# Performance work log

Hardware: AMD Instinct MI355X
Metric: run time of the kernel (lower is better)

The kernel has to match this reference:

```python
import jax, jax.numpy as jnp
import numpy as np

DIM = 1024
HEADS = 16
HEAD_DIM = DIM // HEADS
HIDDEN = int(DIM * 4.0)
EPS = 1e-5


def layernorm(x, w, b):
    m = jnp.mean(x, axis=-1, keepdims=True)
    v = jnp.var(x, axis=-1, keepdims=True)
    return (x - m) * jax.lax.rsqrt(v + EPS) * w + b


def apply_rope(t, pos):
    # t: [B, H, S, D], pos: [B, S] int
    half = t.shape[-1] // 2
    inv_freq = 1.0 / (10000.0 ** (jnp.arange(half, dtype=jnp.float32) / half))
    ang = pos.astype(jnp.float32)[:, None, :, None] * inv_freq  # [B,1,S,half]
    cos = jnp.cos(ang)
    sin = jnp.sin(ang)
    t1, t2 = t[..., :half], t[..., half:]
    return jnp.concatenate([t1 * cos - t2 * sin, t2 * cos + t1 * sin], axis=-1)


def setup_inputs() -> dict:
    key = jax.random.key(0)
    ks = jax.random.split(key, 10)
    B, S = 2, 2048
    x = jax.random.normal(ks[0], (B, S, DIM), dtype=jnp.float32)
    pos = jnp.sort(jax.random.randint(ks[1], (B, S), 0, 2048), axis=-1).astype(jnp.int32)
    def lin(k, fi, fo):
        return jax.random.normal(k, (fi, fo), dtype=jnp.float32) / np.sqrt(fi)
    return {
        "x": x,
        "pos": pos,
        "ln1_w": jnp.ones((DIM,), jnp.float32),
        "ln1_b": jnp.zeros((DIM,), jnp.float32),
        "qkv_w": lin(ks[2], DIM, 3 * DIM),
        "qkv_b": jnp.zeros((3 * DIM,), jnp.float32),
        "o_w": lin(ks[3], DIM, DIM),
        "o_b": jnp.zeros((DIM,), jnp.float32),
        "ln2_w": jnp.ones((DIM,), jnp.float32),
        "ln2_b": jnp.zeros((DIM,), jnp.float32),
        "mlp_w1": lin(ks[4], DIM, HIDDEN),
        "mlp_b1": jnp.zeros((HIDDEN,), jnp.float32),
        "mlp_w2": lin(ks[5], HIDDEN, DIM),
        "mlp_b2": jnp.zeros((DIM,), jnp.float32),
    }


def reference(x, pos, ln1_w, ln1_b, qkv_w, qkv_b, o_w, o_b, ln2_w, ln2_b, mlp_w1, mlp_b1, mlp_w2, mlp_b2):
    B, S, C = x.shape
    scale = HEAD_DIM ** -0.5
    xn = layernorm(x, ln1_w, ln1_b)
    qkv = (xn @ qkv_w + qkv_b).reshape(B, S, 3, HEADS, HEAD_DIM)
    qkv = jnp.transpose(qkv, (2, 0, 3, 1, 4))  # [3,B,H,S,D]
    q, k, v = qkv[0], qkv[1], qkv[2]
    q = apply_rope(q, pos)
    k = apply_rope(k, pos)
    scores = jnp.einsum("bhsd,bhtd->bhst", q, k) * scale
    probs = jax.nn.softmax(scores, axis=-1)
    attn = jnp.einsum("bhst,bhtd->bhsd", probs, v)
    attn = jnp.transpose(attn, (0, 2, 1, 3)).reshape(B, S, C)
    x = x + attn @ o_w + o_b
    xn2 = layernorm(x, ln2_w, ln2_b)
    h = jax.nn.gelu(xn2 @ mlp_w1 + mlp_b1, approximate=False)
    x = x + h @ mlp_w2 + mlp_b2
    return x
```

## Files before the change

### kernel.cpp

```cpp
#include <hip/hip_runtime.h>
#include <hip/hip_bf16.h>
#include <math.h>

#define DIMC 1024
#define HEADS 16
#define HD 64
#define HIDDEN 4096
#define BATCH 2
#define SEQ 2048
#define TOK (BATCH*SEQ)

typedef unsigned short u16;
typedef __attribute__((ext_vector_type(8))) short short8;
typedef __attribute__((ext_vector_type(4))) float f32x4;

__device__ __forceinline__ u16 f2bf(float f) {
  unsigned u = __float_as_uint(f);
  u += 0x7fff + ((u >> 16) & 1);
  return (u16)(u >> 16);
}
__device__ __forceinline__ float bf2f(u16 h) {
  return __uint_as_float(((unsigned)h) << 16);
}

__device__ __forceinline__ void gl_lds16(const void* g, void* l) {
  __builtin_amdgcn_global_load_lds(
      (__attribute__((address_space(1))) void*)g,
      (__attribute__((address_space(3))) void*)l, 16, 0, 0);
}

__device__ __forceinline__ const short8* lds_row128(const u16* base, int row, int chunk) {
  return (const short8*)((const char*)base + row * 128 + (((chunk) ^ (row & 7)) << 4));
}

__global__ __launch_bounds__(256) void ln_kernel(
    const float* __restrict__ x, const float* __restrict__ w,
    const float* __restrict__ b, u16* __restrict__ out)
{
  int row = blockIdx.x, tid = threadIdx.x;
  const float4* xr = (const float4*)(x + (size_t)row * DIMC);
  float4 v = xr[tid];
  float s = v.x + v.y + v.z + v.w;
  float s2 = v.x*v.x + v.y*v.y + v.z*v.z + v.w*v.w;
  for (int off = 32; off > 0; off >>= 1) {
    s  += __shfl_down(s, off);
    s2 += __shfl_down(s2, off);
  }
  __shared__ float red[8];
  int lane = tid & 63, wv = tid >> 6;
  if (lane == 0) { red[wv] = s; red[4 + wv] = s2; }
  __syncthreads();
  float S  = red[0] + red[1] + red[2] + red[3];
  float S2 = red[4] + red[5] + red[6] + red[7];
  float mean = S * (1.f / DIMC);
  float var  = S2 * (1.f / DIMC) - mean * mean;
  float inv  = rsqrtf(var + 1e-5f);
  int base = tid * 4;
  float vv[4] = {v.x, v.y, v.z, v.w};
#pragma unroll
  for (int j = 0; j < 4; ++j)
    out[(size_t)row * DIMC + base + j] = f2bf((vv[j] - mean) * inv * w[base + j] + b[base + j]);
}

__global__ __launch_bounds__(256) void transpose_cast(
    const float* __restrict__ W, u16* __restrict__ Wt, int K, int N)
{
  __shared__ float t[32][33];
  int n0 = blockIdx.x * 32, k0 = blockIdx.y * 32;
  for (int r = threadIdx.y; r < 32; r += 8)
    t[r][threadIdx.x] = W[(size_t)(k0 + r) * N + n0 + threadIdx.x];
  __syncthreads();
  for (int r = threadIdx.y; r < 32; r += 8)
    Wt[(size_t)(n0 + r) * K + k0 + threadIdx.x] = f2bf(t[threadIdx.x][r]);
}

__device__ __forceinline__ void grid_map(int BM, int& m0, int& n0) {
  int gx = gridDim.x, gy = gridDim.y;
  int nwg = gx * gy;
  int orig = blockIdx.y * gx + blockIdx.x;
  int wg = (orig & 7) * (nwg >> 3) + (orig >> 3);
  int bx = wg / gy, by = wg - bx * gy;
  m0 = by * BM;
  n0 = bx * 128;
}

template<int GELU>
__device__ __forceinline__ void gemm_lin_body(
    u16* shm, const u16* __restrict__ A, const u16* __restrict__ Bt,
    const float* __restrict__ bias, u16* __restrict__ outb, int M, int N, int K)
{
  int tid = threadIdx.x;
  int lane = tid & 63, w = tid >> 6;
  int wr = w >> 1, wc = w & 1;
  int m0, n0;
  grid_map(128, m0, n0);

  f32x4 acc[4][4] = {};

  int offA[4], offB[4];
#pragma unroll
  for (int j = 0; j < 4; ++j) {
    int p = tid + j * 256, row = p >> 3, cl = (p & 7) ^ (row & 7);
    offA[j] = (m0 + row) * K + cl * 8;
    offB[j] = (n0 + row) * K + cl * 8;
  }
  int rofs = lane & 15, q4 = lane >> 4;
  int NT = K >> 6;
  u16* Bs = shm + 128 * 64;

  for (int t = 0; t < NT; ++t) {
#pragma unroll
    for (int j = 0; j < 4; ++j) {
      gl_lds16(A + offA[j] + t * 64, shm + (tid + j * 256) * 8);
      gl_lds16(Bt + offB[j] + t * 64, Bs + (tid + j * 256) * 8);
    }
    __syncthreads();
    {
      short8 af[4][2], bfr[4][2];
#pragma unroll
      for (int mm = 0; mm < 4; ++mm)
#pragma unroll
        for (int kk = 0; kk < 2; ++kk) {
          int row = wr * 64 + mm * 16 + rofs;
          af[mm][kk] = *(const short8*)((const char*)shm + row * 128 +
                                        ((((kk << 2) | q4) ^ (row & 7)) << 4));
        }
#pragma unroll
      for (int nn = 0; nn < 4; ++nn)
#pragma unroll
        for (int kk = 0; kk < 2; ++kk) {
          int row = wc * 64 + nn * 16 + rofs;
          bfr[nn][kk] = *(const short8*)((const char*)Bs + row * 128 +
                                         ((((kk << 2) | q4) ^ (row & 7)) << 4));
        }
#pragma unroll
      for (int kk = 0; kk < 2; ++kk)
#pragma unroll
        for (int mm = 0; mm < 4; ++mm)
#pragma unroll
          for (int nn = 0; nn < 4; ++nn)
            acc[mm][nn] = __builtin_amdgcn_mfma_f32_16x16x32_bf16(
                af[mm][kk], bfr[nn][kk], acc[mm][nn], 0, 0, 0);
    }
    __syncthreads();
  }

  u16* C = shm;
#pragma unroll
  for (int nn = 0; nn < 4; ++nn) {
    int ccol = wc * 64 + nn * 16 + rofs;
    float bv = bias[n0 + ccol];
#pragma unroll
    for (int mm = 0; mm < 4; ++mm)
#pragma unroll
      for (int r = 0; r < 4; ++r) {
        int crow = wr * 64 + mm * 16 + q4 * 4 + r;
        float v = acc[mm][nn][r] + bv;
        if (GELU) v = 0.5f * v * (1.f + erff(v * 0.70710678118f));
        C[crow * 128 + ccol] = f2bf(v);
      }
  }
  __syncthreads();
  for (int c = tid; c < 128 * 16; c += 256) {
    int row = c >> 4, off = (c & 15) * 8;
    *(short8*)(outb + (size_t)(m0 + row) * N + n0 + off) = *(const short8*)&C[row * 128 + off];
  }
}

__global__ __launch_bounds__(256) void gemm_qkv(
    const u16* __restrict__ A, const u16* __restrict__ Bt,
    const float* __restrict__ bias, u16* __restrict__ outb, int M, int N, int K)
{
  __shared__ u16 shm[128 * 64 * 2];
  gemm_lin_body<0>(shm, A, Bt, bias, outb, M, N, K);
}
__global__ __launch_bounds__(256) void gemm_mlp1(
    const u16* __restrict__ A, const u16* __restrict__ Bt,
    const float* __restrict__ bias, u16* __restrict__ outb, int M, int N, int K)
{
  __shared__ u16 shm[128 * 64 * 2];
  gemm_lin_body<1>(shm, A, Bt, bias, outb, M, N, K);
}

__device__ __forceinline__ void gemm_res_body(
    u16* shm, const u16* __restrict__ A, const u16* __restrict__ Bt,
    const float* __restrict__ bias, const float* __restrict__ res,
    float* __restrict__ outf, int M, int N, int K)
{
  constexpr int BM = 64, AMM = 2, HALF = 32, AJ = 2;
  constexpr int ASZ = BM * 64, BSZ = 128 * 64;
  int tid = threadIdx.x;
  int lane = tid & 63, w = tid >> 6;
  int wr = w >> 1, wc = w & 1;
  int m0, n0;
  grid_map(BM, m0, n0);

  f32x4 acc[AMM][4] = {};

  int offA[AJ], offB[4];
#pragma unroll
  for (int j = 0; j < AJ; ++j) {
    int p = tid + j * 256, row = p >> 3, cl = (p & 7) ^ (row & 7);
    offA[j] = (m0 + row) * K + cl * 8;
  }
#pragma unroll
  for (int j = 0; j < 4; ++j) {
    int p = tid + j * 256, row = p >> 3, cl = (p & 7) ^ (row & 7);
    offB[j] = (n0 + row) * K + cl * 8;
  }
  int rofs = lane & 15, q4 = lane >> 4;
  int NT = K >> 6;

  auto stage = [&](int buf, int t) {
    u16* Ab = shm + buf * ASZ;
    u16* Bb = shm + 2 * ASZ + buf * BSZ;
#pragma unroll
    for (int j = 0; j < AJ; ++j)
      gl_lds16(A + offA[j] + t * 64, Ab + (tid + j * 256) * 8);
#pragma unroll
    for (int j = 0; j < 4; ++j)
      gl_lds16(Bt + offB[j] + t * 64, Bb + (tid + j * 256) * 8);
  };
  auto compute = [&](int buf) {
    const char* Ab = (const char*)(shm + buf * ASZ);
    const char* Bb = (const char*)(shm + 2 * ASZ + buf * BSZ);
    short8 af[AMM][2], bfr[4][2];
#pragma unroll
    for (int mm = 0; mm < AMM; ++mm)
#pragma unroll
      for (int kk = 0; kk < 2; ++kk) {
        int row = wr * HALF + mm * 16 + rofs;
        af[mm][kk] = *(const short8*)(Ab + row * 128 +
                                      ((((kk << 2) | q4) ^ (row & 7)) << 4));
      }
#pragma unroll
    for (int nn = 0; nn < 4; ++nn)
#pragma unroll
      for (int kk = 0; kk < 2; ++kk) {
        int row = wc * 64 + nn * 16 + rofs;
        bfr[nn][kk] = *(const short8*)(Bb + row * 128 +
                                       ((((kk << 2) | q4) ^ (row & 7)) << 4));
      }
#pragma unroll
    for (int kk = 0; kk < 2; ++kk)
#pragma unroll
      for (int mm = 0; mm < AMM; ++mm)
#pragma unroll
        for (int nn = 0; nn < 4; ++nn)
          acc[mm][nn] = __builtin_amdgcn_mfma_f32_16x16x32_bf16(
              af[mm][kk], bfr[nn][kk], acc[mm][nn], 0, 0, 0);
  };

  stage(0, 0);
  __syncthreads();
  int cur = 0;
  for (int t = 0; t < NT; ++t) {
    if (t + 1 < NT) stage(cur ^ 1, t + 1);
    compute(cur);
    __syncthreads();
    cur ^= 1;
  }

  float* Cf = (float*)shm;
#pragma unroll
  for (int p = 0; p < 2; ++p) {
    if (wr == p) {
#pragma unroll
      for (int nn = 0; nn < 4; ++nn) {
        int ccol = wc * 64 + nn * 16 + rofs;
        float bv = bias[n0 + ccol];
#pragma unroll
        for (int mm = 0; mm < AMM; ++mm)
#pragma unroll
          for (int r = 0; r < 4; ++r)
            Cf[(mm * 16 + q4 * 4 + r) * 128 + ccol] = acc[mm][nn][r] + bv;
      }
    }
    __syncthreads();
    for (int c = tid; c < HALF * 32; c += 256) {
      int row = c >> 5, off = (c & 31) * 4;
      size_t idx = (size_t)(m0 + p * HALF + row) * N + n0 + off;
      float4 rv = *(const float4*)(res + idx);
      float4 cv = *(const float4*)&Cf[row * 128 + off];
      cv.x += rv.x; cv.y += rv.y; cv.z += rv.z; cv.w += rv.w;
      *(float4*)(outf + idx) = cv;
    }
    __syncthreads();
  }
}

__global__ __launch_bounds__(256) void gemm_oproj(
    const u16* __restrict__ A, const u16* __restrict__ Bt,
    const float* __restrict__ bias, const float* __restrict__ res,
    float* __restrict__ outf, int M, int N, int K)
{
  __shared__ u16 shm[(64 + 128) * 64 * 2];
  gemm_res_body(shm, A, Bt, bias, res, outf, M, N, K);
}
__global__ __launch_bounds__(256) void gemm_mlp2(
    const u16* __restrict__ A, const u16* __restrict__ Bt,
    const float* __restrict__ bias, const float* __restrict__ res,
    float* __restrict__ outf, int M, int N, int K)
{
  __shared__ u16 shm[(64 + 128) * 64 * 2];
  gemm_res_body(shm, A, Bt, bias, res, outf, M, N, K);
}

__global__ __launch_bounds__(256) void rope_split(
    const u16* __restrict__ qkv, const int* __restrict__ pos,
    u16* __restrict__ Q, u16* __restrict__ Kk, u16* __restrict__ Vt)
{
  int st = blockIdx.x, bh = blockIdx.y;
  int b = bh >> 4, hh = bh & 15;
  int s0 = st * 64;
  int tid = threadIdx.x;
  __shared__ u16 vtile[64][72];

  for (int i = tid; i < 64 * 32; i += 256) {
    int sl = i >> 5, dp = i & 31;
    int s = s0 + sl;
    float p = (float)pos[b * SEQ + s];
    float freq = exp2f((float)dp * -0.4152410118609203f);
    float ang = p * freq;
    float sn, c;
    __sincosf(ang, &sn, &c);
    const u16* qr = qkv + (size_t)(b * SEQ + s) * 3072 + hh * 64;
    float q1 = bf2f(qr[dp]),        q2 = bf2f(qr[dp + 32]);
    float k1 = bf2f(qr[1024 + dp]), k2 = bf2f(qr[1024 + dp + 32]);
    size_t ob = ((size_t)bh * SEQ + s) * HD;
    const float QS = 0.18033688011112042f;
    Q[ob + dp]       = f2bf((q1 * c - q2 * sn) * QS);
    Q[ob + dp + 32]  = f2bf((q2 * c + q1 * sn) * QS);
    Kk[ob + dp]      = f2bf(k1 * c - k2 * sn);
    Kk[ob + dp + 32] = f2bf(k2 * c + k1 * sn);
  }
  for (int i = tid; i < 64 * 64; i += 256) {
    int sl = i >> 6, d = i & 63;
    vtile[d][sl] = qkv[(size_t)(b * SEQ + s0 + sl) * 3072 + 2048 + hh * 64 + d];
  }
  __syncthreads();
  for (int i = tid; i < 64 * 64; i += 256) {
    int d = i >> 6, sl = i & 63;
    Vt[((size_t)bh * HD + d) * SEQ + s0 + sl] = vtile[d][sl];
  }
}

__global__ __launch_bounds__(256) void attn128(
    const u16* __restrict__ Q, const u16* __restrict__ K,
    const u16* __restrict__ Vt, u16* __restrict__ O)
{
  __shared__ u16 Ks[2][64 * 64];
  __shared__ u16 Vs[2][64 * 64];
  __shared__ u16 Ps[4 * 32 * 64];
  int orig = blockIdx.y * gridDim.x + blockIdx.x;
  int bh = (orig & 7) * 4 + ((orig >> 3) & 3);
  int qt = orig >> 5;
  int b = bh >> 4, hh = bh & 15;
  const u16* Qp = Q + ((size_t)bh * SEQ + qt * 128) * HD;
  const u16* Kp = K + (size_t)bh * SEQ * HD;
  const u16* Vp = Vt + (size_t)bh * HD * SEQ;
  int tid = threadIdx.x, lane = tid & 63, w = tid >> 6;
  int rofs = lane & 15, q4 = lane >> 4;
  int kofs = q4 * 8;

  short8 aq[2][2];
#pragma unroll
  for (int m = 0; m < 2; ++m)
#pragma unroll
    for (int h = 0; h < 2; ++h)
      aq[m][h] = *(const short8*)&Qp[(m * 64 + w * 16 + rofs) * HD + h * 32 + kofs];

  short8 ones;
#pragma unroll
  for (int j = 0; j < 8; ++j) ones[j] = (short)0x3F80;

  f32x4 o[2][4] = {};
  f32x4 lsum[2] = {};

  int srow = tid >> 3;
  int sg0 = ((tid & 7) ^ (srow & 7)) * 8;
  u16* pw = &Ps[w * 32 * 64];

#define A_STAGE(BUF, T0) do { \
    gl_lds16(Kp + (size_t)((T0) + srow) * HD + sg0, &Ks[BUF][tid * 8]); \
    gl_lds16(Kp + (size_t)((T0) + 32 + srow) * HD + sg0, &Ks[BUF][tid * 8 + 2048]); \
    gl_lds16(Vp + (size_t)srow * SEQ + (T0) + sg0, &Vs[BUF][tid * 8]); \
    gl_lds16(Vp + (size_t)(32 + srow) * SEQ + (T0) + sg0, &Vs[BUF][tid * 8 + 2048]); \
  } while (0)

  auto tile = [&](const u16* KsB, const u16* VsB) {
    f32x4 s[2][4] = {};
    short8 bk0[4], bk1[4];
#pragma unroll
    for (int n = 0; n < 4; ++n) {
      int krow = n * 16 + rofs;
      bk0[n] = *lds_row128(KsB, krow, q4);
      bk1[n] = *lds_row128(KsB, krow, 4 + q4);
    }
#pragma unroll
    for (int m = 0; m < 2; ++m)
#pragma unroll
      for (int n = 0; n < 4; ++n) {
        s[m][n] = __builtin_amdgcn_mfma_f32_16x16x32_bf16(aq[m][0], bk0[n], s[m][n], 0, 0, 0);
        s[m][n] = __builtin_amdgcn_mfma_f32_16x16x32_bf16(aq[m][1], bk1[n], s[m][n], 0, 0, 0);
      }
#pragma unroll
    for (int m = 0; m < 2; ++m)
#pragma unroll
      for (int n = 0; n < 4; ++n)
#pragma unroll
        for (int r = 0; r < 4; ++r) {
          int prow = m * 16 + q4 * 4 + r;
          int pbyte = (n * 16 + rofs) * 2;
          float p = __builtin_amdgcn_exp2f(s[m][n][r]);
          *(u16*)((char*)pw + prow * 128 + (pbyte ^ ((prow & 7) << 4))) = f2bf(p);
        }
    short8 pa[2][2];
#pragma unroll
    for (int m = 0; m < 2; ++m) {
      pa[m][0] = *lds_row128(pw, m * 16 + rofs, q4);
      pa[m][1] = *lds_row128(pw, m * 16 + rofs, 4 + q4);
    }
    short8 bv0[4], bv1[4];
#pragma unroll
    for (int n = 0; n < 4; ++n) {
      int vrow = n * 16 + rofs;
      bv0[n] = *lds_row128(VsB, vrow, q4);
      bv1[n] = *lds_row128(VsB, vrow, 4 + q4);
    }
#pragma unroll
    for (int m = 0; m < 2; ++m) {
      lsum[m] = __builtin_amdgcn_mfma_f32_16x16x32_bf16(pa[m][0], ones, lsum[m], 0, 0, 0);
      lsum[m] = __builtin_amdgcn_mfma_f32_16x16x32_bf16(pa[m][1], ones, lsum[m], 0, 0, 0);
#pragma unroll
      for (int n = 0; n < 4; ++n) {
        o[m][n] = __builtin_amdgcn_mfma_f32_16x16x32_bf16(pa[m][0], bv0[n], o[m][n], 0, 0, 0);
        o[m][n] = __builtin_amdgcn_mfma_f32_16x16x32_bf16(pa[m][1], bv1[n], o[m][n], 0, 0, 0);
      }
    }
  };

  A_STAGE(0, 0);
  __syncthreads();
  for (int t0 = 0; t0 < SEQ; t0 += 128) {
    if (t0 + 64 < SEQ) A_STAGE(1, t0 + 64);
    tile(Ks[0], Vs[0]);
    __syncthreads();
    if (t0 + 128 < SEQ) A_STAGE(0, t0 + 128);
    tile(Ks[1], Vs[1]);
    __syncthreads();
  }
#undef A_STAGE

#pragma unroll
  for (int m = 0; m < 2; ++m)
#pragma unroll
    for (int r = 0; r < 4; ++r) {
      float inv = 1.f / lsum[m][r];
      int rr = m * 64 + w * 16 + q4 * 4 + r;
#pragma unroll
      for (int n = 0; n < 4; ++n)
        Ps[rr * 64 + n * 16 + rofs] = f2bf(o[m][n][r] * inv);
    }
  __syncthreads();
  for (int c = tid; c < 128 * 8; c += 256) {
    int row = c >> 3, off = (c & 7) * 8;
    int sq = qt * 128 + row;
    *(short8*)(O + ((size_t)b * SEQ + sq) * DIMC + hh * 64 + off) = *(const short8*)&Ps[row * 64 + off];
  }
}

extern "C" void kernel_launch(void* const* d_in, const int* in_sizes, int n_in,
                              void* d_out, int out_size, void* d_ws, size_t ws_size,
                              hipStream_t stream) {
  const float* x     = (const float*)d_in[0];
  const int*   pos   = (const int*)  d_in[1];
  const float* ln1_w = (const float*)d_in[2];
  const float* ln1_b = (const float*)d_in[3];
  const float* qkv_w = (const float*)d_in[4];
  const float* qkv_b = (const float*)d_in[5];
  const float* o_w   = (const float*)d_in[6];
  const float* o_b   = (const float*)d_in[7];
  const float* ln2_w = (const float*)d_in[8];
  const float* ln2_b = (const float*)d_in[9];
  const float* w1    = (const float*)d_in[10];
  const float* b1    = (const float*)d_in[11];
  const float* w2    = (const float*)d_in[12];
  const float* b2    = (const float*)d_in[13];
  float* out = (float*)d_out;

  char* ws = (char*)d_ws;
  u16* WqkvT = (u16*)(ws + 0);
  u16* WoT   = (u16*)(ws + 6291456);
  u16* W1T   = (u16*)(ws + 8388608);
  u16* W2T   = (u16*)(ws + 16777216);
  u16* xn    = (u16*)(ws + 25165824);
  u16* qkvbf = (u16*)(ws + 33554432);
  u16* Qb    = (u16*)(ws + 58720256);
  u16* Kb    = (u16*)(ws + 67108864);
  u16* Vtb   = (u16*)(ws + 75497472);
  u16* attnb = (u16*)(ws + 83886080);
  u16* hbuf  = (u16*)(ws + 25165824);
  float* x2  = (float*)(ws + 58720256);
  u16* xn2   = (u16*)(ws + 75497472);

  transpose_cast<<<dim3(3072/32, 1024/32), dim3(32, 8), 0, stream>>>(qkv_w, WqkvT, 1024, 3072);
  transpose_cast<<<dim3(1024/32, 1024/32), dim3(32, 8), 0, stream>>>(o_w,  WoT,  1024, 1024);
  transpose_cast<<<dim3(4096/32, 1024/32), dim3(32, 8), 0, stream>>>(w1,   W1T,  1024, 4096);
  transpose_cast<<<dim3(1024/32, 4096/32), dim3(32, 8), 0, stream>>>(w2,   W2T,  4096, 1024);

  ln_kernel<<<TOK, 256, 0, stream>>>(x, ln1_w, ln1_b, xn);
  gemm_qkv<<<dim3(24, 32), 256, 0, stream>>>(xn, WqkvT, qkv_b, qkvbf, 4096, 3072, 1024);
  rope_split<<<dim3(32, 32), 256, 0, stream>>>(qkvbf, pos, Qb, Kb, Vtb);
  attn128<<<dim3(16, 32), 256, 0, stream>>>(Qb, Kb, Vtb, attnb);
  gemm_oproj<<<dim3(8, 64), 256, 0, stream>>>(attnb, WoT, o_b, x, x2, 4096, 1024, 1024);
  ln_kernel<<<TOK, 256, 0, stream>>>(x2, ln2_w, ln2_b, xn2);
  gemm_mlp1<<<dim3(32, 32), 256, 0, stream>>>(xn2, W1T, b1, hbuf, 4096, 4096, 1024);
  gemm_mlp2<<<dim3(8, 64), 256, 0, stream>>>(hbuf, W2T, b2, x2, out, 4096, 1024, 4096);
}
```

Before: 257.6 us.

## Double-buffer QKV GEMM and retile MLP1 GEMM to 256x256 with 1024 threads

The QKV GEMM now uses double-buffered LDS staging, so the next K-tile's global-to-LDS loads overlap the current tile's MFMA work and one barrier per iteration goes away. The MLP1 GEMM is rewritten as a 1024-thread, 256x256 output tile with K-step 32, double buffering and s_setprio around the MFMA block, and its epilogue is written in two halves through LDS. The larger tile is meant to raise operand reuse and cut global traffic. In exchange LDS use and per-block resources grow, and only 256 blocks are launched, which may fill the CUs poorly.

```diff
diff --git a/kernel.cpp b/kernel.cpp
--- a/kernel.cpp
+++ b/kernel.cpp
@@ -74,26 +74,28 @@
     Wt[(size_t)(n0 + r) * K + k0 + threadIdx.x] = f2bf(t[threadIdx.x][r]);
 }
 
-__device__ __forceinline__ void grid_map(int BM, int& m0, int& n0) {
+__device__ __forceinline__ void grid_map(int BM, int BN, int& m0, int& n0) {
   int gx = gridDim.x, gy = gridDim.y;
   int nwg = gx * gy;
   int orig = blockIdx.y * gx + blockIdx.x;
   int wg = (orig & 7) * (nwg >> 3) + (orig >> 3);
   int bx = wg / gy, by = wg - bx * gy;
   m0 = by * BM;
-  n0 = bx * 128;
-}
-
-template<int GELU>
-__device__ __forceinline__ void gemm_lin_body(
-    u16* shm, const u16* __restrict__ A, const u16* __restrict__ Bt,
-    const float* __restrict__ bias, u16* __restrict__ outb, int M, int N, int K)
-{
+  n0 = bx * BN;
+}
+
+__global__ __launch_bounds__(256) void gemm_qkv(
+    const u16* __restrict__ A, const u16* __restrict__ Bt,
+    const float* __restrict__ bias, u16* __restrict__ outb,
+    int M, int N, int K)
+{
+  constexpr int ASZ = 128 * 64, BSZ = 128 * 64;
+  __shared__ u16 shm[ASZ * 2 + BSZ * 2];
   int tid = threadIdx.x;
   int lane = tid & 63, w = tid >> 6;
   int wr = w >> 1, wc = w & 1;
   int m0, n0;
-  grid_map(128, m0, n0);
+  grid_map(128, 128, m0, n0);
 
   f32x4 acc[4][4] = {};
 
@@ -106,43 +108,54 @@
   }
   int rofs = lane & 15, q4 = lane >> 4;
   int NT = K >> 6;
-  u16* Bs = shm + 128 * 64;
-
+
+  auto stage = [&](int buf, int t) {
+    u16* Ab = shm + buf * ASZ;
+    u16* Bb = shm + 2 * ASZ + buf * BSZ;
+#pragma unroll
+    for (int j = 0; j < 4; ++j) {
+      gl_lds16(A + offA[j] + t * 64, Ab + (tid + j * 256) * 8);
+      gl_lds16(Bt + offB[j] + t * 64, Bb + (tid + j * 256) * 8);
+    }
+  };
+  auto compute = [&](int buf) {
+    const char* Ab = (const char*)(shm + buf * ASZ);
+    const char* Bb = (const char*)(shm + 2 * ASZ + buf * BSZ);
+    short8 af[4][2], bfr[4][2];
+#pragma unroll
+    for (int mm = 0; mm < 4; ++mm)
+#pragma unroll
+      for (int kk = 0; kk < 2; ++kk) {
+        int row = wr * 64 + mm * 16 + rofs;
+        af[mm][kk] = *(const short8*)(Ab + row * 128 +
+                                      ((((kk << 2) | q4) ^ (row & 7)) << 4));
+      }
+#pragma unroll
+    for (int nn = 0; nn < 4; ++nn)
+#pragma unroll
+      for (int kk = 0; kk < 2; ++kk) {
+        int row = wc * 64 + nn * 16 + rofs;
+        bfr[nn][kk] = *(const short8*)(Bb + row * 128 +
+                                       ((((kk << 2) | q4) ^ (row & 7)) << 4));
+      }
+#pragma unroll
+    for (int kk = 0; kk < 2; ++kk)
+#pragma unroll
+      for (int mm = 0; mm < 4; ++mm)
+#pragma unroll
+        for (int nn = 0; nn < 4; ++nn)
+          acc[mm][nn] = __builtin_amdgcn_mfma_f32_16x16x32_bf16(
+              af[mm][kk], bfr[nn][kk], acc[mm][nn], 0, 0, 0);
+  };
+
+  stage(0, 0);
+  __syncthreads();
+  int cur = 0;
   for (int t = 0; t < NT; ++t) {
-#pragma unroll
-    for (int j = 0; j < 4; ++j) {
-      gl_lds16(A + offA[j] + t * 64, shm + (tid + j * 256) * 8);
-      gl_lds16(Bt + offB[j] + t * 64, Bs + (tid + j * 256) * 8);
-    }
-    __syncthreads();
-    {
-      short8 af[4][2], bfr[4][2];
-#pragma unroll
-      for (int mm = 0; mm < 4; ++mm)
-#pragma unroll
-        for (int kk = 0; kk < 2; ++kk) {
-          int row = wr * 64 + mm * 16 + rofs;
-          af[mm][kk] = *(const short8*)((const char*)shm + row * 128 +
-                                        ((((kk << 2) | q4) ^ (row & 7)) << 4));
-        }
-#pragma unroll
-      for (int nn = 0; nn < 4; ++nn)
-#pragma unroll
-        for (int kk = 0; kk < 2; ++kk) {
-          int row = wc * 64 + nn * 16 + rofs;
-          bfr[nn][kk] = *(const short8*)((const char*)Bs + row * 128 +
-                                         ((((kk << 2) | q4) ^ (row & 7)) << 4));
-        }
-#pragma unroll
-      for (int kk = 0; kk < 2; ++kk)
-#pragma unroll
-        for (int mm = 0; mm < 4; ++mm)
-#pragma unroll
-          for (int nn = 0; nn < 4; ++nn)
-            acc[mm][nn] = __builtin_amdgcn_mfma_f32_16x16x32_bf16(
-                af[mm][kk], bfr[nn][kk], acc[mm][nn], 0, 0, 0);
-    }
-    __syncthreads();
+    if (t + 1 < NT) stage(cur ^ 1, t + 1);
+    compute(cur);
+    __syncthreads();
+    cur ^= 1;
   }
 
   u16* C = shm;
@@ -155,9 +168,7 @@
 #pragma unroll
       for (int r = 0; r < 4; ++r) {
         int crow = wr * 64 + mm * 16 + q4 * 4 + r;
-        float v = acc[mm][nn][r] + bv;
-        if (GELU) v = 0.5f * v * (1.f + erff(v * 0.70710678118f));
-        C[crow * 128 + ccol] = f2bf(v);
+        C[crow * 128 + ccol] = f2bf(acc[mm][nn][r] + bv);
       }
   }
   __syncthreads();
@@ -167,19 +178,93 @@
   }
 }
 
-__global__ __launch_bounds__(256) void gemm_qkv(
+__global__ __launch_bounds__(1024, 4) void gemm_mlp1(
     const u16* __restrict__ A, const u16* __restrict__ Bt,
-    const float* __restrict__ bias, u16* __restrict__ outb, int M, int N, int K)
-{
-  __shared__ u16 shm[128 * 64 * 2];
-  gemm_lin_body<0>(shm, A, Bt, bias, outb, M, N, K);
-}
-__global__ __launch_bounds__(256) void gemm_mlp1(
-    const u16* __restrict__ A, const u16* __restrict__ Bt,
-    const float* __restrict__ bias, u16* __restrict__ outb, int M, int N, int K)
-{
-  __shared__ u16 shm[128 * 64 * 2];
-  gemm_lin_body<1>(shm, A, Bt, bias, outb, M, N, K);
+    const float* __restrict__ bias, u16* __restrict__ outb,
+    int M, int N, int K)
+{
+  constexpr int BSZ = 256 * 32;
+  __shared__ u16 shm[BSZ * 4];
+  int tid = threadIdx.x;
+  int lane = tid & 63, wid = tid >> 6;
+  int wr = wid >> 2, wn = wid & 3;
+  int rofs = lane & 15, q4 = lane >> 4;
+  int m0, n0;
+  grid_map(256, 256, m0, n0);
+
+  f32x4 acc[4][4] = {};
+
+  int srow = tid >> 2;
+  int slc = (tid & 3) ^ ((srow >> 1) & 3);
+  size_t aoff = (size_t)(m0 + srow) * K + slc * 8;
+  size_t boff = (size_t)(n0 + srow) * K + slc * 8;
+
+  int NT = K >> 5;
+  auto stage = [&](int buf, int t) {
+    gl_lds16(A + aoff + t * 32, shm + buf * BSZ + tid * 8);
+    gl_lds16(Bt + boff + t * 32, shm + (2 + buf) * BSZ + tid * 8);
+  };
+  auto comp = [&](int buf) {
+    const char* Ab = (const char*)(shm + buf * BSZ);
+    const char* Bb = (const char*)(shm + (2 + buf) * BSZ);
+    short8 af[4], bfr[4];
+#pragma unroll
+    for (int mm = 0; mm < 4; ++mm) {
+      int row = wr * 64 + mm * 16 + rofs;
+      af[mm] = *(const short8*)(Ab + row * 64 + ((q4 ^ ((row >> 1) & 3)) << 4));
+    }
+#pragma unroll
+    for (int nn = 0; nn < 4; ++nn) {
+      int row = wn * 64 + nn * 16 + rofs;
+      bfr[nn] = *(const short8*)(Bb + row * 64 + ((q4 ^ ((row >> 1) & 3)) << 4));
+    }
+    __builtin_amdgcn_s_setprio(1);
+#pragma unroll
+    for (int mm = 0; mm < 4; ++mm)
+#pragma unroll
+      for (int nn = 0; nn < 4; ++nn)
+        acc[mm][nn] = __builtin_amdgcn_mfma_f32_16x16x32_bf16(
+            af[mm], bfr[nn], acc[mm][nn], 0, 0, 0);
+    __builtin_amdgcn_s_setprio(0);
+  };
+
+  stage(0, 0);
+  __syncthreads();
+  int cur = 0;
+  for (int t = 0; t < NT; ++t) {
+    if (t + 1 < NT) stage(cur ^ 1, t + 1);
+    comp(cur);
+    __syncthreads();
+    cur ^= 1;
+  }
+
+  u16* Ct = shm;
+#pragma unroll
+  for (int p = 0; p < 2; ++p) {
+    if ((wr >> 1) == p) {
+#pragma unroll
+      for (int nn = 0; nn < 4; ++nn) {
+        int ccol = wn * 64 + nn * 16 + rofs;
+        float bv = bias[n0 + ccol];
+#pragma unroll
+        for (int mm = 0; mm < 4; ++mm)
+#pragma unroll
+          for (int r = 0; r < 4; ++r) {
+            int rl = (wr & 1) * 64 + mm * 16 + q4 * 4 + r;
+            float v = acc[mm][nn][r] + bv;
+            v = 0.5f * v * (1.f + erff(v * 0.70710678118f));
+            Ct[rl * 256 + ccol] = f2bf(v);
+          }
+      }
+    }
+    __syncthreads();
+    for (int c = tid; c < 128 * 32; c += 1024) {
+      int row = c >> 5, off = (c & 31) * 8;
+      *(short8*)(outb + (size_t)(m0 + p * 128 + row) * N + n0 + off) =
+          *(const short8*)&Ct[row * 256 + off];
+    }
+    __syncthreads();
+  }
 }
 
 __device__ __forceinline__ void gemm_res_body(
@@ -193,7 +278,7 @@
   int lane = tid & 63, w = tid >> 6;
   int wr = w >> 1, wc = w & 1;
   int m0, n0;
-  grid_map(BM, m0, n0);
+  grid_map(BM, 128, m0, n0);
 
   f32x4 acc[AMM][4] = {};
 
@@ -515,6 +600,6 @@
   attn128<<<dim3(16, 32), 256, 0, stream>>>(Qb, Kb, Vtb, attnb);
   gemm_oproj<<<dim3(8, 64), 256, 0, stream>>>(attnb, WoT, o_b, x, x2, 4096, 1024, 1024);
   ln_kernel<<<TOK, 256, 0, stream>>>(x2, ln2_w, ln2_b, xn2);
-  gemm_mlp1<<<dim3(32, 32), 256, 0, stream>>>(xn2, W1T, b1, hbuf, 4096, 4096, 1024);
+  gemm_mlp1<<<dim3(16, 16), 1024, 0, stream>>>(xn2, W1T, b1, hbuf, 4096, 4096, 1024);
   gemm_mlp2<<<dim3(8, 64), 256, 0, stream>>>(hbuf, W2T, b2, x2, out, 4096, 1024, 4096);
 }
```

Result: slower. 312.5 us (+21.3%).

## Pad operand leading dimensions and double-buffer the linear GEMM main loop

Applied to the files above, without the earlier changes.

Intermediate bf16 buffers (normalized activations, transposed weights, attention output, MLP hidden, transposed V) get padded row strides (1088, 4128, 2112 elements) so that power-of-two strides no longer map rows onto the same memory channels or cache sets. The QKV and MLP1 GEMM gains a two-stage LDS double buffer, so the next K-tile's global-to-LDS load overlaps the current tile's MFMA work and one barrier per iteration goes away. The double buffer doubles that kernel's LDS use, which may cut occupancy, and the workspace offsets are reshuffled to fit the larger padded buffers.

```diff
diff --git a/kernel.cpp b/kernel.cpp
--- a/kernel.cpp
+++ b/kernel.cpp
@@ -10,6 +10,10 @@
 #define SEQ 2048
 #define TOK (BATCH*SEQ)
 
+#define LDP 1088
+#define LDH 4128
+#define LDV 2112
+
 typedef unsigned short u16;
 typedef __attribute__((ext_vector_type(8))) short short8;
 typedef __attribute__((ext_vector_type(4))) float f32x4;
@@ -35,7 +39,7 @@
 
 __global__ __launch_bounds__(256) void ln_kernel(
     const float* __restrict__ x, const float* __restrict__ w,
-    const float* __restrict__ b, u16* __restrict__ out)
+    const float* __restrict__ b, u16* __restrict__ out, int ostr)
 {
   int row = blockIdx.x, tid = threadIdx.x;
   const float4* xr = (const float4*)(x + (size_t)row * DIMC);
@@ -59,11 +63,11 @@
   float vv[4] = {v.x, v.y, v.z, v.w};
 #pragma unroll
   for (int j = 0; j < 4; ++j)
-    out[(size_t)row * DIMC + base + j] = f2bf((vv[j] - mean) * inv * w[base + j] + b[base + j]);
+    out[(size_t)row * ostr + base + j] = f2bf((vv[j] - mean) * inv * w[base + j] + b[base + j]);
 }
 
 __global__ __launch_bounds__(256) void transpose_cast(
-    const float* __restrict__ W, u16* __restrict__ Wt, int K, int N)
+    const float* __restrict__ W, u16* __restrict__ Wt, int K, int N, int ldo)
 {
   __shared__ float t[32][33];
   int n0 = blockIdx.x * 32, k0 = blockIdx.y * 32;
@@ -71,29 +75,32 @@
     t[r][threadIdx.x] = W[(size_t)(k0 + r) * N + n0 + threadIdx.x];
   __syncthreads();
   for (int r = threadIdx.y; r < 32; r += 8)
-    Wt[(size_t)(n0 + r) * K + k0 + threadIdx.x] = f2bf(t[threadIdx.x][r]);
-}
-
-__device__ __forceinline__ void grid_map(int BM, int& m0, int& n0) {
+    Wt[(size_t)(n0 + r) * ldo + k0 + threadIdx.x] = f2bf(t[threadIdx.x][r]);
+}
+
+__device__ __forceinline__ void grid_map(int BM, int BN, int& m0, int& n0) {
   int gx = gridDim.x, gy = gridDim.y;
   int nwg = gx * gy;
   int orig = blockIdx.y * gx + blockIdx.x;
   int wg = (orig & 7) * (nwg >> 3) + (orig >> 3);
   int bx = wg / gy, by = wg - bx * gy;
   m0 = by * BM;
-  n0 = bx * 128;
+  n0 = bx * BN;
 }
 
 template<int GELU>
-__device__ __forceinline__ void gemm_lin_body(
-    u16* shm, const u16* __restrict__ A, const u16* __restrict__ Bt,
-    const float* __restrict__ bias, u16* __restrict__ outb, int M, int N, int K)
+__global__ __launch_bounds__(256) void gemm_lin(
+    const u16* __restrict__ A, const u16* __restrict__ Bt,
+    const float* __restrict__ bias, u16* __restrict__ outb,
+    int M, int N, int K, int lda, int ldb, int ldc)
 {
+  constexpr int ASZ = 128 * 64, BSZ = 128 * 64;
+  __shared__ u16 shm[ASZ * 2 + BSZ * 2];
   int tid = threadIdx.x;
   int lane = tid & 63, w = tid >> 6;
   int wr = w >> 1, wc = w & 1;
   int m0, n0;
-  grid_map(128, m0, n0);
+  grid_map(128, 128, m0, n0);
 
   f32x4 acc[4][4] = {};
 
@@ -101,48 +108,59 @@
 #pragma unroll
   for (int j = 0; j < 4; ++j) {
     int p = tid + j * 256, row = p >> 3, cl = (p & 7) ^ (row & 7);
-    offA[j] = (m0 + row) * K + cl * 8;
-    offB[j] = (n0 + row) * K + cl * 8;
+    offA[j] = (m0 + row) * lda + cl * 8;
+    offB[j] = (n0 + row) * ldb + cl * 8;
   }
   int rofs = lane & 15, q4 = lane >> 4;
   int NT = K >> 6;
-  u16* Bs = shm + 128 * 64;
-
+
+  auto stage = [&](int buf, int t) {
+    u16* Ab = shm + buf * ASZ;
+    u16* Bb = shm + 2 * ASZ + buf * BSZ;
+#pragma unroll
+    for (int j = 0; j < 4; ++j) {
+      gl_lds16(A + offA[j] + t * 64, Ab + (tid + j * 256) * 8);
+      gl_lds16(Bt + offB[j] + t * 64, Bb + (tid + j * 256) * 8);
+    }
+  };
+  auto compute = [&](int buf) {
+    const char* Ab = (const char*)(shm + buf * ASZ);
+    const char* Bb = (const char*)(shm + 2 * ASZ + buf * BSZ);
+    short8 af[4][2], bfr[4][2];
+#pragma unroll
+    for (int mm = 0; mm < 4; ++mm)
+#pragma unroll
+      for (int kk = 0; kk < 2; ++kk) {
+        int row = wr * 64 + mm * 16 + rofs;
+        af[mm][kk] = *(const short8*)(Ab + row * 128 +
+                                      ((((kk << 2) | q4) ^ (row & 7)) << 4));
+      }
+#pragma unroll
+    for (int nn = 0; nn < 4; ++nn)
+#pragma unroll
+      for (int kk = 0; kk < 2; ++kk) {
+        int row = wc * 64 + nn * 16 + rofs;
+        bfr[nn][kk] = *(const short8*)(Bb + row * 128 +
+                                       ((((kk << 2) | q4) ^ (row & 7)) << 4));
+      }
+#pragma unroll
+    for (int kk = 0; kk < 2; ++kk)
+#pragma unroll
+      for (int mm = 0; mm < 4; ++mm)
+#pragma unroll
+        for (int nn = 0; nn < 4; ++nn)
+          acc[mm][nn] = __builtin_amdgcn_mfma_f32_16x16x32_bf16(
+              af[mm][kk], bfr[nn][kk], acc[mm][nn], 0, 0, 0);
+  };
+
+  stage(0, 0);
+  __syncthreads();
+  int cur = 0;
   for (int t = 0; t < NT; ++t) {
-#pragma unroll
-    for (int j = 0; j < 4; ++j) {
-      gl_lds16(A + offA[j] + t * 64, shm + (tid + j * 256) * 8);
-      gl_lds16(Bt + offB[j] + t * 64, Bs + (tid + j * 256) * 8);
-    }
+    if (t + 1 < NT) stage(cur ^ 1, t + 1);
+    compute(cur);
     __syncthreads();
-    {
-      short8 af[4][2], bfr[4][2];
-#pragma unroll
-      for (int mm = 0; mm < 4; ++mm)
-#pragma unroll
-        for (int kk = 0; kk < 2; ++kk) {
-          int row = wr * 64 + mm * 16 + rofs;
-          af[mm][kk] = *(const short8*)((const char*)shm + row * 128 +
-                                        ((((kk << 2) | q4) ^ (row & 7)) << 4));
-        }
-#pragma unroll
-      for (int nn = 0; nn < 4; ++nn)
-#pragma unroll
-        for (int kk = 0; kk < 2; ++kk) {
-          int row = wc * 64 + nn * 16 + rofs;
-          bfr[nn][kk] = *(const short8*)((const char*)Bs + row * 128 +
-                                         ((((kk << 2) | q4) ^ (row & 7)) << 4));
-        }
-#pragma unroll
-      for (int kk = 0; kk < 2; ++kk)
-#pragma unroll
-        for (int mm = 0; mm < 4; ++mm)
-#pragma unroll
-          for (int nn = 0; nn < 4; ++nn)
-            acc[mm][nn] = __builtin_amdgcn_mfma_f32_16x16x32_bf16(
-                af[mm][kk], bfr[nn][kk], acc[mm][nn], 0, 0, 0);
-    }
-    __syncthreads();
+    cur ^= 1;
   }
 
   u16* C = shm;
@@ -163,37 +181,23 @@
   __syncthreads();
   for (int c = tid; c < 128 * 16; c += 256) {
     int row = c >> 4, off = (c & 15) * 8;
-    *(short8*)(outb + (size_t)(m0 + row) * N + n0 + off) = *(const short8*)&C[row * 128 + off];
-  }
-}
-
-__global__ __launch_bounds__(256) void gemm_qkv(
+    *(short8*)(outb + (size_t)(m0 + row) * ldc + n0 + off) = *(const short8*)&C[row * 128 + off];
+  }
+}
+
+__global__ __launch_bounds__(256) void gemm_res(
     const u16* __restrict__ A, const u16* __restrict__ Bt,
-    const float* __restrict__ bias, u16* __restrict__ outb, int M, int N, int K)
-{
-  __shared__ u16 shm[128 * 64 * 2];
-  gemm_lin_body<0>(shm, A, Bt, bias, outb, M, N, K);
-}
-__global__ __launch_bounds__(256) void gemm_mlp1(
-    const u16* __restrict__ A, const u16* __restrict__ Bt,
-    const float* __restrict__ bias, u16* __restrict__ outb, int M, int N, int K)
-{
-  __shared__ u16 shm[128 * 64 * 2];
-  gemm_lin_body<1>(shm, A, Bt, bias, outb, M, N, K);
-}
-
-__device__ __forceinline__ void gemm_res_body(
-    u16* shm, const u16* __restrict__ A, const u16* __restrict__ Bt,
     const float* __restrict__ bias, const float* __restrict__ res,
-    float* __restrict__ outf, int M, int N, int K)
+    float* __restrict__ outf, int M, int N, int K, int lda, int ldb)
 {
   constexpr int BM = 64, AMM = 2, HALF = 32, AJ = 2;
   constexpr int ASZ = BM * 64, BSZ = 128 * 64;
+  __shared__ u16 shm[(BM + 128) * 64 * 2];
   int tid = threadIdx.x;
   int lane = tid & 63, w = tid >> 6;
   int wr = w >> 1, wc = w & 1;
   int m0, n0;
-  grid_map(BM, m0, n0);
+  grid_map(BM, 128, m0, n0);
 
   f32x4 acc[AMM][4] = {};
 
@@ -201,12 +205,12 @@
 #pragma unroll
   for (int j = 0; j < AJ; ++j) {
     int p = tid + j * 256, row = p >> 3, cl = (p & 7) ^ (row & 7);
-    offA[j] = (m0 + row) * K + cl * 8;
+    offA[j] = (m0 + row) * lda + cl * 8;
   }
 #pragma unroll
   for (int j = 0; j < 4; ++j) {
     int p = tid + j * 256, row = p >> 3, cl = (p & 7) ^ (row & 7);
-    offB[j] = (n0 + row) * K + cl * 8;
+    offB[j] = (n0 + row) * ldb + cl * 8;
   }
   int rofs = lane & 15, q4 = lane >> 4;
   int NT = K >> 6;
@@ -287,23 +291,6 @@
     }
     __syncthreads();
   }
-}
-
-__global__ __launch_bounds__(256) void gemm_oproj(
-    const u16* __restrict__ A, const u16* __restrict__ Bt,
-    const float* __restrict__ bias, const float* __restrict__ res,
-    float* __restrict__ outf, int M, int N, int K)
-{
-  __shared__ u16 shm[(64 + 128) * 64 * 2];
-  gemm_res_body(shm, A, Bt, bias, res, outf, M, N, K);
-}
-__global__ __launch_bounds__(256) void gemm_mlp2(
-    const u16* __restrict__ A, const u16* __restrict__ Bt,
-    const float* __restrict__ bias, const float* __restrict__ res,
-    float* __restrict__ outf, int M, int N, int K)
-{
-  __shared__ u16 shm[(64 + 128) * 64 * 2];
-  gemm_res_body(shm, A, Bt, bias, res, outf, M, N, K);
 }
 
 __global__ __launch_bounds__(256) void rope_split(
@@ -341,7 +328,7 @@
   __syncthreads();
   for (int i = tid; i < 64 * 64; i += 256) {
     int d = i >> 6, sl = i & 63;
-    Vt[((size_t)bh * HD + d) * SEQ + s0 + sl] = vtile[d][sl];
+    Vt[((size_t)bh * HD + d) * LDV + s0 + sl] = vtile[d][sl];
   }
 }
 
@@ -358,7 +345,7 @@
   int b = bh >> 4, hh = bh & 15;
   const u16* Qp = Q + ((size_t)bh * SEQ + qt * 128) * HD;
   const u16* Kp = K + (size_t)bh * SEQ * HD;
-  const u16* Vp = Vt + (size_t)bh * HD * SEQ;
+  const u16* Vp = Vt + (size_t)bh * HD * LDV;
   int tid = threadIdx.x, lane = tid & 63, w = tid >> 6;
   int rofs = lane & 15, q4 = lane >> 4;
   int kofs = q4 * 8;
@@ -384,8 +371,8 @@
 #define A_STAGE(BUF, T0) do { \
     gl_lds16(Kp + (size_t)((T0) + srow) * HD + sg0, &Ks[BUF][tid * 8]); \
     gl_lds16(Kp + (size_t)((T0) + 32 + srow) * HD + sg0, &Ks[BUF][tid * 8 + 2048]); \
-    gl_lds16(Vp + (size_t)srow * SEQ + (T0) + sg0, &Vs[BUF][tid * 8]); \
-    gl_lds16(Vp + (size_t)(32 + srow) * SEQ + (T0) + sg0, &Vs[BUF][tid * 8 + 2048]); \
+    gl_lds16(Vp + (size_t)srow * LDV + (T0) + sg0, &Vs[BUF][tid * 8]); \
+    gl_lds16(Vp + (size_t)(32 + srow) * LDV + (T0) + sg0, &Vs[BUF][tid * 8 + 2048]); \
   } while (0)
 
   auto tile = [&](const u16* KsB, const u16* VsB) {
@@ -466,7 +453,7 @@
   for (int c = tid; c < 128 * 8; c += 256) {
     int row = c >> 3, off = (c & 7) * 8;
     int sq = qt * 128 + row;
-    *(short8*)(O + ((size_t)b * SEQ + sq) * DIMC + hh * 64 + off) = *(const short8*)&Ps[row * 64 + off];
+    *(short8*)(O + ((size_t)b * SEQ + sq) * LDP + hh * 64 + off) = *(const short8*)&Ps[row * 64 + off];
   }
 }
 
@@ -491,30 +478,30 @@
 
   char* ws = (char*)d_ws;
   u16* WqkvT = (u16*)(ws + 0);
-  u16* WoT   = (u16*)(ws + 6291456);
-  u16* W1T   = (u16*)(ws + 8388608);
-  u16* W2T   = (u16*)(ws + 16777216);
-  u16* xn    = (u16*)(ws + 25165824);
-  u16* qkvbf = (u16*)(ws + 33554432);
-  u16* Qb    = (u16*)(ws + 58720256);
-  u16* Kb    = (u16*)(ws + 67108864);
-  u16* Vtb   = (u16*)(ws + 75497472);
-  u16* attnb = (u16*)(ws + 83886080);
-  u16* hbuf  = (u16*)(ws + 25165824);
-  float* x2  = (float*)(ws + 58720256);
-  u16* xn2   = (u16*)(ws + 75497472);
-
-  transpose_cast<<<dim3(3072/32, 1024/32), dim3(32, 8), 0, stream>>>(qkv_w, WqkvT, 1024, 3072);
-  transpose_cast<<<dim3(1024/32, 1024/32), dim3(32, 8), 0, stream>>>(o_w,  WoT,  1024, 1024);
-  transpose_cast<<<dim3(4096/32, 1024/32), dim3(32, 8), 0, stream>>>(w1,   W1T,  1024, 4096);
-  transpose_cast<<<dim3(1024/32, 4096/32), dim3(32, 8), 0, stream>>>(w2,   W2T,  4096, 1024);
-
-  ln_kernel<<<TOK, 256, 0, stream>>>(x, ln1_w, ln1_b, xn);
-  gemm_qkv<<<dim3(24, 32), 256, 0, stream>>>(xn, WqkvT, qkv_b, qkvbf, 4096, 3072, 1024);
+  u16* WoT   = (u16*)(ws + 6684672);
+  u16* W1T   = (u16*)(ws + 8912896);
+  u16* W2T   = (u16*)(ws + 17825792);
+  u16* xn    = (u16*)(ws + 26279936);
+  u16* qkvbf = (u16*)(ws + 35192832);
+  u16* Qb    = (u16*)(ws + 60358656);
+  u16* Kb    = (u16*)(ws + 68747264);
+  u16* Vtb   = (u16*)(ws + 77135872);
+  u16* attnb = (u16*)(ws + 35192832);
+  float* x2  = (float*)(ws + 60358656);
+  u16* xn2   = (u16*)(ws + 77135872);
+  u16* hbuf  = (u16*)(ws + 26279936);
+
+  transpose_cast<<<dim3(3072/32, 1024/32), dim3(32, 8), 0, stream>>>(qkv_w, WqkvT, 1024, 3072, LDP);
+  transpose_cast<<<dim3(1024/32, 1024/32), dim3(32, 8), 0, stream>>>(o_w,  WoT,  1024, 1024, LDP);
+  transpose_cast<<<dim3(4096/32, 1024/32), dim3(32, 8), 0, stream>>>(w1,   W1T,  1024, 4096, LDP);
+  transpose_cast<<<dim3(1024/32, 4096/32), dim3(32, 8), 0, stream>>>(w2,   W2T,  4096, 1024, LDH);
+
+  ln_kernel<<<TOK, 256, 0, stream>>>(x, ln1_w, ln1_b, xn, LDP);
+  gemm_lin<0><<<dim3(24, 32), 256, 0, stream>>>(xn, WqkvT, qkv_b, qkvbf, 4096, 3072, 1024, LDP, LDP, 3072);
   rope_split<<<dim3(32, 32), 256, 0, stream>>>(qkvbf, pos, Qb, Kb, Vtb);
   attn128<<<dim3(16, 32), 256, 0, stream>>>(Qb, Kb, Vtb, attnb);
-  gemm_oproj<<<dim3(8, 64), 256, 0, stream>>>(attnb, WoT, o_b, x, x2, 4096, 1024, 1024);
-  ln_kernel<<<TOK, 256, 0, stream>>>(x2, ln2_w, ln2_b, xn2);
-  gemm_mlp1<<<dim3(32, 32), 256, 0, stream>>>(xn2, W1T, b1, hbuf, 4096, 4096, 1024);
-  gemm_mlp2<<<dim3(8, 64), 256, 0, stream>>>(hbuf, W2T, b2, x2, out, 4096, 1024, 4096);
-}
+  gemm_res<<<dim3(8, 64), 256, 0, stream>>>(attnb, WoT, o_b, x, x2, 4096, 1024, 1024, LDP, LDP);
+  ln_kernel<<<TOK, 256, 0, stream>>>(x2, ln2_w, ln2_b, xn2, LDP);
+  gemm_lin<1><<<dim3(32, 32), 256, 0, stream>>>(xn2, W1T, b1, hbuf, 4096, 4096, 1024, LDP, LDP, LDH);
+  gemm_res<<<dim3(8, 64), 256, 0, stream>>>(hbuf, W2T, b2, x2, out, 4096, 1024, 4096, LDH, LDH);
+}
```

Result: slower. 273.5 us (+6.2%).
